# Kernel optimization log

Measured on AMD Instinct MI355X. Metric: run time of the kernel, lower is better.

The kernel has to match this reference:

```python
import jax, jax.numpy as jnp
import numpy as np

S_FACTOR = 2          # scale_factor
GRID = 64             # coarse grid side -> M = 64^3 coarse voxels
C_IN = 32
C_MID = 32
C_OUT = 256


def setup_inputs() -> dict:
    key = jax.random.key(0)
    k1, k2, k3 = jax.random.split(key, 3)
    s = S_FACTOR
    S = s ** 3
    M = GRID ** 3
    # coarse voxel coords in canonical (lexicographic) order
    r = jnp.arange(GRID)
    ci, cj, ck = jnp.meshgrid(r, r, r, indexing='ij')
    coarse = jnp.stack([ci.ravel(), cj.ravel(), ck.ravel()], axis=-1)  # (M, 3)
    lo = jnp.arange(s)
    li, lj, lk = jnp.meshgrid(lo, lo, lo, indexing='ij')
    local = jnp.stack([li.ravel(), lj.ravel(), lk.ravel()], axis=-1)   # (S, 3)
    # fine voxel coords: every coarse voxel fully occupied -> N = M*S
    ijk = (coarse[:, None, :] * s + local[None, :, :]).reshape(M * S, 3).astype(jnp.int32)
    # ijk_to_index on the coarse grid (precomputed grid lookup, int constant)
    down_index = jnp.repeat(jnp.arange(M, dtype=jnp.int32), S)
    in_data = jax.random.normal(k1, (M * S, C_IN), dtype=jnp.float32)
    W_mid = jax.random.normal(k2, (C_IN, C_MID), dtype=jnp.float32) / np.sqrt(C_IN).astype(np.float32)
    W_out = jax.random.normal(k3, (C_MID * S, C_OUT), dtype=jnp.float32) / np.sqrt(C_MID * S).astype(np.float32)
    return {"in_data": in_data, "W_mid": W_mid, "W_out": W_out,
            "ijk": ijk, "down_index": down_index, "num_coarse": M}


def reference(in_data, W_mid, W_out, ijk, down_index, num_coarse):
    s = S_FACTOR
    S = s ** 3
    # middle_proj (LinearFVDB, bias=False)
    x = in_data @ W_mid                                   # (N, C_mid)
    C = x.shape[1]
    # local coordinate within the s^3 block (floor division; ijk >= 0 here)
    down_ijk = ijk // s
    local = ijk - down_ijk * s                            # (N, 3) in [0, s)
    local_index = local[:, 0] * (s * s) + local[:, 1] * s + local[:, 2]
    flat_idx = down_index.astype(jnp.int32) * S + local_index.astype(jnp.int32)
    # scatter_add into zero buffer (mapping is a unique permutation)
    flat_target = jnp.zeros((num_coarse * S, C), dtype=x.dtype).at[flat_idx].add(x)
    down_data = flat_target.reshape(num_coarse, S * C)    # (M, S*C)
    # out_proj (LinearFVDB, bias=False)
    return down_data @ W_out                              # (M, C_out)
```

## Files before the change

### kernel.cpp

```cpp
#include <hip/hip_runtime.h>
#include <hip/hip_bf16.h>


typedef short bf16x8 __attribute__((ext_vector_type(8)));
typedef float f32x4 __attribute__((ext_vector_type(4)));

__device__ __forceinline__ unsigned short f2bf(float f) {
    union { float f; unsigned u; } x; x.f = f;
    unsigned u = x.u;
    u += 0x7fffu + ((u >> 16) & 1u);
    return (unsigned short)(u >> 16);
}

__global__ void build_wf(const float* __restrict__ Wmid,
                         const float* __restrict__ Wout,
                         unsigned short* __restrict__ Wt) {
    const int o = blockIdx.x;
    const int k = threadIdx.x;
    const int s = k >> 5;
    const int j = k & 31;
    float acc = 0.f;
#pragma unroll
    for (int c = 0; c < 32; ++c)
        acc += Wmid[j * 32 + c] * Wout[(s * 32 + c) * 256 + o];
    Wt[o * 256 + k] = f2bf(acc);
}

__global__ __launch_bounds__(256, 4) void gemm_fused(
    const float* __restrict__ A,
    const unsigned short* __restrict__ Wt,
    float* __restrict__ out)
{
    __shared__ __align__(16) unsigned short Abuf[64 * 256];

    const int t = threadIdx.x;
    const long m0 = (long)blockIdx.x * 64;

    const int wave = t >> 6;
    const int lane = t & 63;
    const int q    = lane >> 4;
    const int r16  = lane & 15;

    const float* abase_g = A + m0 * 256;
    float4 va[16];
#pragma unroll
    for (int i = 0; i < 8; ++i) {
        const float* src = abase_g + (long)(i * 256 + t) * 8;
        va[2 * i]     = *(const float4*)(src);
        va[2 * i + 1] = *(const float4*)(src + 4);
    }
#pragma unroll
    for (int i = 0; i < 8; ++i) {
        int ch  = i * 256 + t;
        int row = ch >> 5;
        int sub = ch & 31;
        bf16x8 b;
        b[0] = (short)f2bf(va[2 * i].x);     b[1] = (short)f2bf(va[2 * i].y);
        b[2] = (short)f2bf(va[2 * i].z);     b[3] = (short)f2bf(va[2 * i].w);
        b[4] = (short)f2bf(va[2 * i + 1].x); b[5] = (short)f2bf(va[2 * i + 1].y);
        b[6] = (short)f2bf(va[2 * i + 1].z); b[7] = (short)f2bf(va[2 * i + 1].w);
        unsigned off = (unsigned)(row * 512 + sub * 16) ^ (unsigned)((row & 7) << 4);
        *(bf16x8*)((char*)Abuf + off) = b;
    }

    const unsigned short* wbase = Wt + (long)(wave * 64 + r16) * 256 + q * 8;
    bf16x8 bcur[4];
#pragma unroll
    for (int nt = 0; nt < 4; ++nt)
        bcur[nt] = *(const bf16x8*)(wbase + nt * 4096);

    f32x4 acc[4][4];
#pragma unroll
    for (int i = 0; i < 4; ++i)
#pragma unroll
        for (int j = 0; j < 4; ++j)
            acc[i][j] = (f32x4){0.f, 0.f, 0.f, 0.f};

    __syncthreads();

    const unsigned abase = (unsigned)(r16 * 512 + q * 16);
    const unsigned aswz  = (unsigned)((r16 & 7) << 4);

#pragma unroll
    for (int kb = 0; kb < 8; ++kb) {
        bf16x8 bnxt[4];
        if (kb < 7) {
#pragma unroll
            for (int nt = 0; nt < 4; ++nt)
                bnxt[nt] = *(const bf16x8*)(wbase + nt * 4096 + (kb + 1) * 32);
        }
        bf16x8 af[4];
#pragma unroll
        for (int mt = 0; mt < 4; ++mt)
            af[mt] = *(const bf16x8*)((const char*)Abuf +
                      (((unsigned)(mt * 8192 + kb * 64) + abase) ^ aswz));
#pragma unroll
        for (int mt = 0; mt < 4; ++mt)
#pragma unroll
            for (int nt = 0; nt < 4; ++nt)
                acc[mt][nt] = __builtin_amdgcn_mfma_f32_16x16x32_bf16(
                    af[mt], bcur[nt], acc[mt][nt], 0, 0, 0);
        if (kb < 7) {
#pragma unroll
            for (int nt = 0; nt < 4; ++nt)
                bcur[nt] = bnxt[nt];
        }
    }

#pragma unroll
    for (int mt = 0; mt < 4; ++mt)
#pragma unroll
        for (int nt = 0; nt < 4; ++nt)
#pragma unroll
            for (int rg = 0; rg < 4; ++rg) {
                int row = mt * 16 + q * 4 + rg;
                int col = wave * 64 + nt * 16 + r16;
                out[(m0 + row) * 256 + col] = acc[mt][nt][rg];
            }
}

extern "C" void kernel_launch(void* const* d_in, const int* in_sizes, int n_in,
                              void* d_out, int out_size, void* d_ws, size_t ws_size,
                              hipStream_t stream) {
    const float* in_data = (const float*)d_in[0];
    const float* W_mid   = (const float*)d_in[1];
    const float* W_out   = (const float*)d_in[2];

    const int Nf = in_sizes[0] / 32;
    const int M  = Nf / 8;

    unsigned short* Wt = (unsigned short*)d_ws;

    build_wf<<<256, 256, 0, stream>>>(W_mid, W_out, Wt);
    gemm_fused<<<M / 64, 256, 0, stream>>>(in_data, Wt, (float*)d_out);
}
```

Before: 489.9 us.

## Make GEMM persistent with double-buffered async global-to-LDS A loads

Turns the fused GEMM into a multi-tile loop: each block handles 8 tiles of 32 rows and keeps the full B fragment set in registers. A is copied into double-buffered LDS with global_load_lds (fp32, swizzled) so the next tile's load overlaps the current tile's MFMAs, and bf16 conversion moves to the LDS-read path. This removes the per-block serial load-convert-compute sequence and the repeated weight loads. The cost is larger LDS (64KB), more registers, lower occupancy, and a grid of only 1024 blocks.

```diff
diff --git a/kernel.cpp b/kernel.cpp
--- a/kernel.cpp
+++ b/kernel.cpp
@@ -26,97 +26,107 @@
     Wt[o * 256 + k] = f2bf(acc);
 }
 
-__global__ __launch_bounds__(256, 4) void gemm_fused(
+__device__ __forceinline__ void gld16(const void* g, void* l) {
+    __builtin_amdgcn_global_load_lds(
+        (const __attribute__((address_space(1))) void*)g,
+        (__attribute__((address_space(3))) void*)l, 16, 0, 0);
+}
+
+__device__ __forceinline__ bf16x8 cvt8(f32x4 lo, f32x4 hi) {
+    union { __hip_bfloat162 h2[4]; bf16x8 v; } u;
+    u.h2[0] = __float22bfloat162_rn(make_float2(lo[0], lo[1]));
+    u.h2[1] = __float22bfloat162_rn(make_float2(lo[2], lo[3]));
+    u.h2[2] = __float22bfloat162_rn(make_float2(hi[0], hi[1]));
+    u.h2[3] = __float22bfloat162_rn(make_float2(hi[2], hi[3]));
+    return u.v;
+}
+
+#define BM 32
+#define TILE_BYTES (BM * 1024)
+#define TPB 8
+
+__global__ __launch_bounds__(256, 2) void gemm_fused(
     const float* __restrict__ A,
     const unsigned short* __restrict__ Wt,
     float* __restrict__ out)
 {
-    __shared__ __align__(16) unsigned short Abuf[64 * 256];
+    __shared__ __align__(16) float Abuf[2][BM * 256];
 
-    const int t = threadIdx.x;
-    const long m0 = (long)blockIdx.x * 64;
-
+    const int t    = threadIdx.x;
     const int wave = t >> 6;
     const int lane = t & 63;
     const int q    = lane >> 4;
     const int r16  = lane & 15;
 
-    const float* abase_g = A + m0 * 256;
-    float4 va[16];
-#pragma unroll
-    for (int i = 0; i < 8; ++i) {
-        const float* src = abase_g + (long)(i * 256 + t) * 8;
-        va[2 * i]     = *(const float4*)(src);
-        va[2 * i + 1] = *(const float4*)(src + 4);
-    }
-#pragma unroll
-    for (int i = 0; i < 8; ++i) {
-        int ch  = i * 256 + t;
-        int row = ch >> 5;
-        int sub = ch & 31;
-        bf16x8 b;
-        b[0] = (short)f2bf(va[2 * i].x);     b[1] = (short)f2bf(va[2 * i].y);
-        b[2] = (short)f2bf(va[2 * i].z);     b[3] = (short)f2bf(va[2 * i].w);
-        b[4] = (short)f2bf(va[2 * i + 1].x); b[5] = (short)f2bf(va[2 * i + 1].y);
-        b[6] = (short)f2bf(va[2 * i + 1].z); b[7] = (short)f2bf(va[2 * i + 1].w);
-        unsigned off = (unsigned)(row * 512 + sub * 16) ^ (unsigned)((row & 7) << 4);
-        *(bf16x8*)((char*)Abuf + off) = b;
-    }
-
-    const unsigned short* wbase = Wt + (long)(wave * 64 + r16) * 256 + q * 8;
-    bf16x8 bcur[4];
+    bf16x8 bs[4][8];
+    const unsigned short* wbase = Wt + (wave * 64 + r16) * 256 + q * 8;
 #pragma unroll
     for (int nt = 0; nt < 4; ++nt)
-        bcur[nt] = *(const bf16x8*)(wbase + nt * 4096);
+#pragma unroll
+        for (int kb = 0; kb < 8; ++kb)
+            bs[nt][kb] = *(const bf16x8*)(wbase + nt * 4096 + kb * 32);
 
-    f32x4 acc[4][4];
+    const long tile0 = (long)blockIdx.x * TPB;
+
+    auto stage = [&](long tt, int buf) {
+        const char* tb = (const char*)A + tt * TILE_BYTES;
 #pragma unroll
-    for (int i = 0; i < 4; ++i)
+        for (int i = 0; i < 8; ++i) {
+            int off  = (i * 256 + t) * 16;
+            int row  = i * 4 + wave;
+            int soff = off ^ ((row & 7) << 4);
+            gld16(tb + soff, (char*)&Abuf[buf][0] + i * 4096 + wave * 1024);
+        }
+    };
+
+    stage(tile0, 0);
+
+    for (int ti = 0; ti < TPB; ++ti) {
+        const long tt = tile0 + ti;
+        __syncthreads();
+
+        if (ti + 1 < TPB) stage(tt + 1, (ti + 1) & 1);
+
+        const char* ab = (const char*)&Abuf[ti & 1][0];
+
+        f32x4 acc[2][4];
 #pragma unroll
-        for (int j = 0; j < 4; ++j)
-            acc[i][j] = (f32x4){0.f, 0.f, 0.f, 0.f};
-
-    __syncthreads();
-
-    const unsigned abase = (unsigned)(r16 * 512 + q * 16);
-    const unsigned aswz  = (unsigned)((r16 & 7) << 4);
+        for (int i = 0; i < 2; ++i)
+#pragma unroll
+            for (int j = 0; j < 4; ++j)
+                acc[i][j] = (f32x4){0.f, 0.f, 0.f, 0.f};
 
 #pragma unroll
-    for (int kb = 0; kb < 8; ++kb) {
-        bf16x8 bnxt[4];
-        if (kb < 7) {
+        for (int kb = 0; kb < 8; ++kb) {
+            bf16x8 af[2];
+#pragma unroll
+            for (int mt = 0; mt < 2; ++mt) {
+                unsigned phys = ((unsigned)((mt * 16 + r16) * 1024 + kb * 128 + q * 32))
+                                ^ ((unsigned)(r16 & 7) << 4);
+                f32x4 lo = *(const f32x4*)(ab + phys);
+                f32x4 hi = *(const f32x4*)(ab + (phys ^ 16u));
+                af[mt] = cvt8(lo, hi);
+            }
+#pragma unroll
+            for (int mt = 0; mt < 2; ++mt)
+#pragma unroll
+                for (int nt = 0; nt < 4; ++nt)
+                    acc[mt][nt] = __builtin_amdgcn_mfma_f32_16x16x32_bf16(
+                        af[mt], bs[nt][kb], acc[mt][nt], 0, 0, 0);
+        }
+
+        float* ob = out + tt * (BM * 256);
+#pragma unroll
+        for (int mt = 0; mt < 2; ++mt)
 #pragma unroll
             for (int nt = 0; nt < 4; ++nt)
-                bnxt[nt] = *(const bf16x8*)(wbase + nt * 4096 + (kb + 1) * 32);
-        }
-        bf16x8 af[4];
 #pragma unroll
-        for (int mt = 0; mt < 4; ++mt)
-            af[mt] = *(const bf16x8*)((const char*)Abuf +
-                      (((unsigned)(mt * 8192 + kb * 64) + abase) ^ aswz));
-#pragma unroll
-        for (int mt = 0; mt < 4; ++mt)
-#pragma unroll
-            for (int nt = 0; nt < 4; ++nt)
-                acc[mt][nt] = __builtin_amdgcn_mfma_f32_16x16x32_bf16(
-                    af[mt], bcur[nt], acc[mt][nt], 0, 0, 0);
-        if (kb < 7) {
-#pragma unroll
-            for (int nt = 0; nt < 4; ++nt)
-                bcur[nt] = bnxt[nt];
-        }
+                for (int rg = 0; rg < 4; ++rg) {
+                    int row = mt * 16 + q * 4 + rg;
+                    int col = wave * 64 + nt * 16 + r16;
+                    ob[row * 256 + col] = acc[mt][nt][rg];
+                }
     }
-
-#pragma unroll
-    for (int mt = 0; mt < 4; ++mt)
-#pragma unroll
-        for (int nt = 0; nt < 4; ++nt)
-#pragma unroll
-            for (int rg = 0; rg < 4; ++rg) {
-                int row = mt * 16 + q * 4 + rg;
-                int col = wave * 64 + nt * 16 + r16;
-                out[(m0 + row) * 256 + col] = acc[mt][nt][rg];
-            }
 }
 
 extern "C" void kernel_launch(void* const* d_in, const int* in_sizes, int n_in,
@@ -132,5 +142,7 @@
     unsigned short* Wt = (unsigned short*)d_ws;
 
     build_wf<<<256, 256, 0, stream>>>(W_mid, W_out, Wt);
-    gemm_fused<<<M / 64, 256, 0, stream>>>(in_data, Wt, (float*)d_out);
+    const int tiles  = M / BM;
+    const int blocks = tiles / TPB;
+    gemm_fused<<<blocks, 256, 0, stream>>>(in_data, Wt, (float*)d_out);
 }
```

After: 465.9 us. 4.9% less time.
